# Kernel optimization log

Measured on AMD Instinct MI355X. Metric: run time of the kernel, lower is better.

The kernel has to match this reference:

```python
import jax, jax.numpy as jnp
import numpy as np

IN_DIM = 2048
H1, H2 = 128, 64
LATENT = 4
KDIM = 1024
GAMMA = 1.0
THRESHOLD = 0.0
BATCH = 65536


def setup_inputs() -> dict:
    key = jax.random.key(0)
    ks = jax.random.split(key, 12)
    s = lambda fan_in: 1.0 / np.sqrt(fan_in)
    inp = {
        "x": jax.random.normal(ks[0], (BATCH, IN_DIM), dtype=jnp.float32),
        # encoder params (stored [in, out]; math x @ W + b)
        "W1": jax.random.uniform(ks[1], (IN_DIM, H1), jnp.float32, -s(IN_DIM), s(IN_DIM)),
        "b1": jnp.zeros((H1,), jnp.float32),
        "W2": jax.random.uniform(ks[2], (H1, H2), jnp.float32, -s(H1), s(H1)),
        "b2": jnp.zeros((H2,), jnp.float32),
        "W3": jax.random.uniform(ks[3], (H2, LATENT), jnp.float32, -s(H2), s(H2)),
        "b3": jnp.zeros((LATENT,), jnp.float32),
        # 2x2 conv filter (flattened kernel) + bias
        "conv_k": jax.random.uniform(ks[4], (LATENT,), jnp.float32, -0.5, 0.5),
        "conv_b": jnp.zeros((), jnp.float32),
        # RBF basis (width LATENT+1: latent features + conv scalar)
        "basis": jax.random.normal(ks[5], (KDIM, LATENT + 1), dtype=jnp.float32),
        "head_w": jax.random.uniform(ks[6], (KDIM,), jnp.float32, -s(KDIM), s(KDIM)),
        "head_b": jnp.zeros((), jnp.float32),
    }
    return inp


def reference(x, W1, b1, W2, b2, W3, b3, conv_k, conv_b, basis, head_w, head_b):
    # encoder (dropout is eval-mode identity)
    h = jax.nn.relu(x @ W1 + b1)
    h = jax.nn.relu(h @ W2 + b2)
    z = h @ W3 + b3                                  # [B, 4]
    # ConvFilter.run on the 2x2 reshape of z: a 2x2 conv over a 2x2 input is a
    # single dot product; mean over the 1x1 output is identity.
    conv_vec = jax.nn.sigmoid(z @ conv_k + conv_b - THRESHOLD)  # [B]
    z = jnp.concatenate([z, conv_vec[:, None]], axis=-1)        # [B, 5]
    # batched RBF kernel to all basis vectors: exp(-gamma * ||z_i - b_j||^2)
    sq = (jnp.sum(z * z, axis=-1, keepdims=True)
          + jnp.sum(basis * basis, axis=-1)[None, :]
          - 2.0 * (z @ basis.T))                     # [B, KDIM]
    k_mat = jnp.exp(-GAMMA * sq)
    out = k_mat @ head_w + head_b                    # [B]
    return out
```

## Files before the change

kernel.cpp:

```cpp
#include <hip/hip_runtime.h>
#include <hip/hip_bf16.h>
#include <math.h>

typedef __attribute__((ext_vector_type(8))) __bf16 bf16x8;
typedef __attribute__((ext_vector_type(4))) float f32x4;

#define IN_DIM 2048
#define NH1 128
#define NH2 64
#define KDIM 1024

__device__ inline f32x4 mfma16(bf16x8 a, bf16x8 b, f32x4 c) {
    return __builtin_amdgcn_mfma_f32_16x16x32_bf16(a, b, c, 0, 0, 0);
}

__global__ void prep_kernel(const float* __restrict__ W1,
                            const float* __restrict__ W2,
                            const float* __restrict__ basis,
                            const float* __restrict__ head_w,
                            __bf16* __restrict__ w1f,
                            __bf16* __restrict__ w2f,
                            float* __restrict__ bp) {
    int idx = blockIdx.x * 256 + threadIdx.x;
    if (idx < IN_DIM * NH1) {
        int ks = idx >> 12;
        int rem = idx & 4095;
        int c = rem >> 9;
        int q = rem & 511;
        int l = q >> 3, e = q & 7;
        int k = ks * 32 + ((l >> 4) << 3) + e;
        int col = (c << 4) + (l & 15);
        w1f[idx] = (__bf16)W1[k * NH1 + col];
    }
    if (idx < NH1 * NH2) {
        int cb = idx >> 9;
        int c2 = cb >> 2, kb = cb & 3;
        int q = idx & 511;
        int l = q >> 3, e = q & 7;
        int k = kb * 32 + ((l >> 4) << 3) + e;
        int col = (c2 << 4) + (l & 15);
        w2f[idx] = (__bf16)W2[k * NH2 + col];
    }
    if (idx < KDIM) {
        const float* b = basis + idx * 5;
        float n2 = b[0]*b[0] + b[1]*b[1] + b[2]*b[2] + b[3]*b[3] + b[4]*b[4];
        float* o = bp + idx * 8;
        o[0] = b[0]; o[1] = b[1]; o[2] = b[2]; o[3] = b[3]; o[4] = b[4];
        o[5] = 1.0f;
        o[6] = head_w[idx] * expf(-n2);
        o[7] = 0.0f;
    }
}

__launch_bounds__(256)
__global__ void fused_main(const float* __restrict__ x,
                           const __bf16* __restrict__ w1f,
                           const float* __restrict__ b1,
                           const __bf16* __restrict__ w2f,
                           const float* __restrict__ b2,
                           const float* __restrict__ W3,
                           const float* __restrict__ b3,
                           const float* __restrict__ conv_k,
                           const float* __restrict__ conv_b,
                           const float* __restrict__ bp,
                           const float* __restrict__ head_b,
                           float* __restrict__ out) {
    __shared__ __bf16 h1s[4][32 * NH1];
    __shared__ float z5s[128][8];
    __shared__ float psum[128];

    const int tid = threadIdx.x;
    const int w = __builtin_amdgcn_readfirstlane(tid >> 6);
    const int l = tid & 63;
    const int row0 = blockIdx.x * 128 + w * 32;

    f32x4 acc[2][8];
#pragma unroll
    for (int g = 0; g < 2; ++g)
#pragma unroll
        for (int c = 0; c < 8; ++c) acc[g][c] = (f32x4){0.f, 0.f, 0.f, 0.f};

    const float* xw0 = x + (size_t)(row0 + (l & 15)) * IN_DIM + ((l >> 4) << 3);
    const float* xw1 = xw0 + (size_t)16 * IN_DIM;
    const __bf16* wbase = w1f + l * 8;

    for (int ks = 0; ks < 64; ++ks) {
        const float* p0 = xw0 + ks * 32;
        const float* p1 = xw1 + ks * 32;
        f32x4 a00 = *(const f32x4*)p0;
        f32x4 a01 = *(const f32x4*)(p0 + 4);
        f32x4 a10 = *(const f32x4*)p1;
        f32x4 a11 = *(const f32x4*)(p1 + 4);
        bf16x8 A0, A1;
        A0[0] = (__bf16)a00.x; A0[1] = (__bf16)a00.y; A0[2] = (__bf16)a00.z; A0[3] = (__bf16)a00.w;
        A0[4] = (__bf16)a01.x; A0[5] = (__bf16)a01.y; A0[6] = (__bf16)a01.z; A0[7] = (__bf16)a01.w;
        A1[0] = (__bf16)a10.x; A1[1] = (__bf16)a10.y; A1[2] = (__bf16)a10.z; A1[3] = (__bf16)a10.w;
        A1[4] = (__bf16)a11.x; A1[5] = (__bf16)a11.y; A1[6] = (__bf16)a11.z; A1[7] = (__bf16)a11.w;
        const __bf16* wp = wbase + ((size_t)ks << 12);
#pragma unroll
        for (int c = 0; c < 8; ++c) {
            bf16x8 B = *(const bf16x8*)(wp + (c << 9));
            acc[0][c] = mfma16(A0, B, acc[0][c]);
            acc[1][c] = mfma16(A1, B, acc[1][c]);
        }
    }

    float b1v[8];
#pragma unroll
    for (int c = 0; c < 8; ++c) b1v[c] = b1[c * 16 + (l & 15)];
    __bf16* hw1 = &h1s[w][0];
#pragma unroll
    for (int g = 0; g < 2; ++g)
#pragma unroll
        for (int c = 0; c < 8; ++c)
#pragma unroll
            for (int r = 0; r < 4; ++r) {
                int rr = g * 16 + ((l >> 4) << 2) + r;
                int cc = c * 16 + (l & 15);
                hw1[rr * NH1 + cc] = (__bf16)fmaxf(acc[g][c][r] + b1v[c], 0.f);
            }

    __syncthreads();

    f32x4 acc2[2][4];
#pragma unroll
    for (int g = 0; g < 2; ++g)
#pragma unroll
        for (int c = 0; c < 4; ++c) acc2[g][c] = (f32x4){0.f, 0.f, 0.f, 0.f};

#pragma unroll
    for (int kb = 0; kb < 4; ++kb) {
        bf16x8 A0 = *(const bf16x8*)&hw1[(l & 15) * NH1 + kb * 32 + ((l >> 4) << 3)];
        bf16x8 A1 = *(const bf16x8*)&hw1[(16 + (l & 15)) * NH1 + kb * 32 + ((l >> 4) << 3)];
#pragma unroll
        for (int c2 = 0; c2 < 4; ++c2) {
            bf16x8 B = *(const bf16x8*)(w2f + (((c2 << 2) + kb) << 9) + l * 8);
            acc2[0][c2] = mfma16(A0, B, acc2[0][c2]);
            acc2[1][c2] = mfma16(A1, B, acc2[1][c2]);
        }
    }

    float b2v[4];
#pragma unroll
    for (int c2 = 0; c2 < 4; ++c2) b2v[c2] = b2[c2 * 16 + (l & 15)];
    float w3l[4][4];
#pragma unroll
    for (int c2 = 0; c2 < 4; ++c2) {
        f32x4 t = *(const f32x4*)&W3[(c2 * 16 + (l & 15)) * 4];
        w3l[c2][0] = t.x; w3l[c2][1] = t.y; w3l[c2][2] = t.z; w3l[c2][3] = t.w;
    }
    float h2v[2][4][4];
#pragma unroll
    for (int g = 0; g < 2; ++g)
#pragma unroll
        for (int c2 = 0; c2 < 4; ++c2)
#pragma unroll
            for (int r = 0; r < 4; ++r)
                h2v[g][c2][r] = fmaxf(acc2[g][c2][r] + b2v[c2], 0.f);

    float pz[2][4][4];
#pragma unroll
    for (int g = 0; g < 2; ++g)
#pragma unroll
        for (int r = 0; r < 4; ++r)
#pragma unroll
            for (int j = 0; j < 4; ++j) {
                float s = 0.f;
#pragma unroll
                for (int c2 = 0; c2 < 4; ++c2) s = fmaf(h2v[g][c2][r], w3l[c2][j], s);
                pz[g][r][j] = s;
            }
#pragma unroll
    for (int off = 1; off < 16; off <<= 1)
#pragma unroll
        for (int g = 0; g < 2; ++g)
#pragma unroll
            for (int r = 0; r < 4; ++r)
#pragma unroll
                for (int j = 0; j < 4; ++j)
                    pz[g][r][j] += __shfl_xor(pz[g][r][j], off, 64);

    const float ck0 = conv_k[0], ck1 = conv_k[1], ck2 = conv_k[2], ck3 = conv_k[3];
    const float cbv = conv_b[0];
    const float b30 = b3[0], b31 = b3[1], b32 = b3[2], b33 = b3[3];
    const float L2E = 1.44269504088896340736f;

    if ((l & 15) == 0) {
#pragma unroll
        for (int g = 0; g < 2; ++g)
#pragma unroll
            for (int r = 0; r < 4; ++r) {
                int rl = w * 32 + g * 16 + ((l >> 4) << 2) + r;
                float z0 = pz[g][r][0] + b30;
                float z1 = pz[g][r][1] + b31;
                float z2 = pz[g][r][2] + b32;
                float z3 = pz[g][r][3] + b33;
                float s = fmaf(z0, ck0, fmaf(z1, ck1, fmaf(z2, ck2, fmaf(z3, ck3, cbv))));
                float sg = 1.f / (1.f + expf(-s));
                float n2 = z0*z0 + z1*z1 + z2*z2 + z3*z3 + sg*sg;
                z5s[rl][0] = 2.f * L2E * z0;
                z5s[rl][1] = 2.f * L2E * z1;
                z5s[rl][2] = 2.f * L2E * z2;
                z5s[rl][3] = 2.f * L2E * z3;
                z5s[rl][4] = 2.f * L2E * sg;
                z5s[rl][5] = -L2E * n2;
            }
    }
    __syncthreads();

    const int row = tid & 127;
    const int half = __builtin_amdgcn_readfirstlane(tid >> 7);
    f32x4 za = *(const f32x4*)&z5s[row][0];
    float z4s = z5s[row][4];
    float z5c = z5s[row][5];
    const float* bpp = bp + (size_t)half * 512 * 8;
    float accum = 0.f;
#pragma unroll 4
    for (int j = 0; j < 512; ++j) {
        f32x4 q0 = *(const f32x4*)&bpp[j * 8];
        f32x4 q1 = *(const f32x4*)&bpp[j * 8 + 4];
        float arg = fmaf(za.x, q0.x,
                    fmaf(za.y, q0.y,
                    fmaf(za.z, q0.z,
                    fmaf(za.w, q0.w,
                    fmaf(z4s, q1.x, z5c)))));
        accum = fmaf(q1.z, exp2f(arg), accum);
    }
    if (half) psum[row] = accum;
    __syncthreads();
    if (!half) out[blockIdx.x * 128 + row] = accum + psum[row] + head_b[0];
}

extern "C" void kernel_launch(void* const* d_in, const int* in_sizes, int n_in,
                              void* d_out, int out_size, void* d_ws, size_t ws_size,
                              hipStream_t stream) {
    const float* x     = (const float*)d_in[0];
    const float* W1    = (const float*)d_in[1];
    const float* b1    = (const float*)d_in[2];
    const float* W2    = (const float*)d_in[3];
    const float* b2    = (const float*)d_in[4];
    const float* W3    = (const float*)d_in[5];
    const float* b3    = (const float*)d_in[6];
    const float* ck    = (const float*)d_in[7];
    const float* cb    = (const float*)d_in[8];
    const float* basis = (const float*)d_in[9];
    const float* hwv   = (const float*)d_in[10];
    const float* hb    = (const float*)d_in[11];

    __bf16* w1f = (__bf16*)d_ws;
    __bf16* w2f = (__bf16*)((char*)d_ws + 524288);
    float*  bpp = (float*)((char*)d_ws + 524288 + 16384);

    prep_kernel<<<1024, 256, 0, stream>>>(W1, W2, basis, hwv, w1f, w2f, bpp);
    fused_main<<<512, 256, 0, stream>>>(x, w1f, b1, w2f, b2, W3, b3, ck, cb,
                                        bpp, hb, (float*)d_out);
}
```

Before: 194.6 us.

## Halve rows per wave, double grid, and software-prefetch x tiles in layer 1

Each wave now handles 16 rows instead of 32, so the grid grows from 512 to 1024 blocks of 64 rows. This cuts accumulator registers, and launch bounds request 4 blocks per CU for higher occupancy. The first GEMM loop is unrolled by two, with the x loads for step ks+2 issued ahead to hide global latency. The RBF stage splits the basis across all four waves with a four-way partial-sum reduction. The trade-off is that each W1 fragment loaded is now reused for half as many rows, so W1 read traffic per output doubles.

```diff
diff --git a/kernel.cpp b/kernel.cpp
--- a/kernel.cpp
+++ b/kernel.cpp
@@ -52,7 +52,27 @@
     }
 }
 
-__launch_bounds__(256)
+
+#define S1_STEP(A0, A1, KS, PF_EN, PA0, PA1, KPF)                             \
+    {                                                                         \
+        bf16x8 Af;                                                            \
+        Af[0] = (__bf16)A0.x; Af[1] = (__bf16)A0.y;                           \
+        Af[2] = (__bf16)A0.z; Af[3] = (__bf16)A0.w;                           \
+        Af[4] = (__bf16)A1.x; Af[5] = (__bf16)A1.y;                           \
+        Af[6] = (__bf16)A1.z; Af[7] = (__bf16)A1.w;                           \
+        if (PF_EN) {                                                          \
+            PA0 = *(const f32x4*)(xp + (KPF) * 32);                           \
+            PA1 = *(const f32x4*)(xp + (KPF) * 32 + 4);                       \
+        }                                                                     \
+        const __bf16* wp = wbase + ((size_t)(KS) << 12);                      \
+        _Pragma("unroll")                                                     \
+        for (int c = 0; c < 8; ++c) {                                         \
+            bf16x8 B = *(const bf16x8*)(wp + (c << 9));                       \
+            acc[c] = mfma16(Af, B, acc[c]);                                   \
+        }                                                                     \
+    }
+
+__launch_bounds__(256, 4)
 __global__ void fused_main(const float* __restrict__ x,
                            const __bf16* __restrict__ w1f,
                            const float* __restrict__ b1,
@@ -65,78 +85,60 @@
                            const float* __restrict__ bp,
                            const float* __restrict__ head_b,
                            float* __restrict__ out) {
-    __shared__ __bf16 h1s[4][32 * NH1];
-    __shared__ float z5s[128][8];
-    __shared__ float psum[128];
+    __shared__ __bf16 h1s[4][16 * NH1];
+    __shared__ __align__(16) float z5s[64][8];
+    __shared__ float psum[4][64];
 
     const int tid = threadIdx.x;
     const int w = __builtin_amdgcn_readfirstlane(tid >> 6);
     const int l = tid & 63;
-    const int row0 = blockIdx.x * 128 + w * 32;
-
-    f32x4 acc[2][8];
-#pragma unroll
-    for (int g = 0; g < 2; ++g)
-#pragma unroll
-        for (int c = 0; c < 8; ++c) acc[g][c] = (f32x4){0.f, 0.f, 0.f, 0.f};
-
-    const float* xw0 = x + (size_t)(row0 + (l & 15)) * IN_DIM + ((l >> 4) << 3);
-    const float* xw1 = xw0 + (size_t)16 * IN_DIM;
+    const int row0 = blockIdx.x * 64 + w * 16;
+
+    f32x4 acc[8];
+#pragma unroll
+    for (int c = 0; c < 8; ++c) acc[c] = (f32x4){0.f, 0.f, 0.f, 0.f};
+
+    const float* xp = x + (size_t)(row0 + (l & 15)) * IN_DIM + ((l >> 4) << 3);
     const __bf16* wbase = w1f + l * 8;
 
-    for (int ks = 0; ks < 64; ++ks) {
-        const float* p0 = xw0 + ks * 32;
-        const float* p1 = xw1 + ks * 32;
-        f32x4 a00 = *(const f32x4*)p0;
-        f32x4 a01 = *(const f32x4*)(p0 + 4);
-        f32x4 a10 = *(const f32x4*)p1;
-        f32x4 a11 = *(const f32x4*)(p1 + 4);
-        bf16x8 A0, A1;
-        A0[0] = (__bf16)a00.x; A0[1] = (__bf16)a00.y; A0[2] = (__bf16)a00.z; A0[3] = (__bf16)a00.w;
-        A0[4] = (__bf16)a01.x; A0[5] = (__bf16)a01.y; A0[6] = (__bf16)a01.z; A0[7] = (__bf16)a01.w;
-        A1[0] = (__bf16)a10.x; A1[1] = (__bf16)a10.y; A1[2] = (__bf16)a10.z; A1[3] = (__bf16)a10.w;
-        A1[4] = (__bf16)a11.x; A1[5] = (__bf16)a11.y; A1[6] = (__bf16)a11.z; A1[7] = (__bf16)a11.w;
-        const __bf16* wp = wbase + ((size_t)ks << 12);
-#pragma unroll
-        for (int c = 0; c < 8; ++c) {
-            bf16x8 B = *(const bf16x8*)(wp + (c << 9));
-            acc[0][c] = mfma16(A0, B, acc[0][c]);
-            acc[1][c] = mfma16(A1, B, acc[1][c]);
-        }
-    }
+    f32x4 aA0 = *(const f32x4*)(xp);
+    f32x4 aA1 = *(const f32x4*)(xp + 4);
+    f32x4 aB0 = *(const f32x4*)(xp + 32);
+    f32x4 aB1 = *(const f32x4*)(xp + 36);
+
+    for (int ks = 0; ks < 62; ks += 2) {
+        S1_STEP(aA0, aA1, ks,     1, aA0, aA1, ks + 2)
+        S1_STEP(aB0, aB1, ks + 1, 1, aB0, aB1, ks + 3)
+    }
+    S1_STEP(aA0, aA1, 62, 0, aA0, aA1, 0)
+    S1_STEP(aB0, aB1, 63, 0, aB0, aB1, 0)
 
     float b1v[8];
 #pragma unroll
     for (int c = 0; c < 8; ++c) b1v[c] = b1[c * 16 + (l & 15)];
     __bf16* hw1 = &h1s[w][0];
 #pragma unroll
-    for (int g = 0; g < 2; ++g)
-#pragma unroll
-        for (int c = 0; c < 8; ++c)
-#pragma unroll
-            for (int r = 0; r < 4; ++r) {
-                int rr = g * 16 + ((l >> 4) << 2) + r;
-                int cc = c * 16 + (l & 15);
-                hw1[rr * NH1 + cc] = (__bf16)fmaxf(acc[g][c][r] + b1v[c], 0.f);
-            }
+    for (int c = 0; c < 8; ++c)
+#pragma unroll
+        for (int r = 0; r < 4; ++r) {
+            int rr = ((l >> 4) << 2) + r;
+            int cc = c * 16 + (l & 15);
+            hw1[rr * NH1 + cc] = (__bf16)fmaxf(acc[c][r] + b1v[c], 0.f);
+        }
 
     __syncthreads();
 
-    f32x4 acc2[2][4];
-#pragma unroll
-    for (int g = 0; g < 2; ++g)
-#pragma unroll
-        for (int c = 0; c < 4; ++c) acc2[g][c] = (f32x4){0.f, 0.f, 0.f, 0.f};
+    f32x4 acc2[4];
+#pragma unroll
+    for (int c2 = 0; c2 < 4; ++c2) acc2[c2] = (f32x4){0.f, 0.f, 0.f, 0.f};
 
 #pragma unroll
     for (int kb = 0; kb < 4; ++kb) {
-        bf16x8 A0 = *(const bf16x8*)&hw1[(l & 15) * NH1 + kb * 32 + ((l >> 4) << 3)];
-        bf16x8 A1 = *(const bf16x8*)&hw1[(16 + (l & 15)) * NH1 + kb * 32 + ((l >> 4) << 3)];
+        bf16x8 A = *(const bf16x8*)&hw1[(l & 15) * NH1 + kb * 32 + ((l >> 4) << 3)];
 #pragma unroll
         for (int c2 = 0; c2 < 4; ++c2) {
             bf16x8 B = *(const bf16x8*)(w2f + (((c2 << 2) + kb) << 9) + l * 8);
-            acc2[0][c2] = mfma16(A0, B, acc2[0][c2]);
-            acc2[1][c2] = mfma16(A1, B, acc2[1][c2]);
+            acc2[c2] = mfma16(A, B, acc2[c2]);
         }
     }
 
@@ -149,36 +151,30 @@
         f32x4 t = *(const f32x4*)&W3[(c2 * 16 + (l & 15)) * 4];
         w3l[c2][0] = t.x; w3l[c2][1] = t.y; w3l[c2][2] = t.z; w3l[c2][3] = t.w;
     }
-    float h2v[2][4][4];
-#pragma unroll
-    for (int g = 0; g < 2; ++g)
-#pragma unroll
-        for (int c2 = 0; c2 < 4; ++c2)
-#pragma unroll
-            for (int r = 0; r < 4; ++r)
-                h2v[g][c2][r] = fmaxf(acc2[g][c2][r] + b2v[c2], 0.f);
-
-    float pz[2][4][4];
-#pragma unroll
-    for (int g = 0; g < 2; ++g)
+    float h2v[4][4];
+#pragma unroll
+    for (int c2 = 0; c2 < 4; ++c2)
 #pragma unroll
         for (int r = 0; r < 4; ++r)
-#pragma unroll
-            for (int j = 0; j < 4; ++j) {
-                float s = 0.f;
-#pragma unroll
-                for (int c2 = 0; c2 < 4; ++c2) s = fmaf(h2v[g][c2][r], w3l[c2][j], s);
-                pz[g][r][j] = s;
-            }
+            h2v[c2][r] = fmaxf(acc2[c2][r] + b2v[c2], 0.f);
+
+    float pz[4][4];
+#pragma unroll
+    for (int r = 0; r < 4; ++r)
+#pragma unroll
+        for (int j = 0; j < 4; ++j) {
+            float s = 0.f;
+#pragma unroll
+            for (int c2 = 0; c2 < 4; ++c2) s = fmaf(h2v[c2][r], w3l[c2][j], s);
+            pz[r][j] = s;
+        }
 #pragma unroll
     for (int off = 1; off < 16; off <<= 1)
 #pragma unroll
-        for (int g = 0; g < 2; ++g)
-#pragma unroll
-            for (int r = 0; r < 4; ++r)
-#pragma unroll
-                for (int j = 0; j < 4; ++j)
-                    pz[g][r][j] += __shfl_xor(pz[g][r][j], off, 64);
+        for (int r = 0; r < 4; ++r)
+#pragma unroll
+            for (int j = 0; j < 4; ++j)
+                pz[r][j] += __shfl_xor(pz[r][j], off, 64);
 
     const float ck0 = conv_k[0], ck1 = conv_k[1], ck2 = conv_k[2], ck3 = conv_k[3];
     const float cbv = conv_b[0];
@@ -187,36 +183,32 @@
 
     if ((l & 15) == 0) {
 #pragma unroll
-        for (int g = 0; g < 2; ++g)
-#pragma unroll
-            for (int r = 0; r < 4; ++r) {
-                int rl = w * 32 + g * 16 + ((l >> 4) << 2) + r;
-                float z0 = pz[g][r][0] + b30;
-                float z1 = pz[g][r][1] + b31;
-                float z2 = pz[g][r][2] + b32;
-                float z3 = pz[g][r][3] + b33;
-                float s = fmaf(z0, ck0, fmaf(z1, ck1, fmaf(z2, ck2, fmaf(z3, ck3, cbv))));
-                float sg = 1.f / (1.f + expf(-s));
-                float n2 = z0*z0 + z1*z1 + z2*z2 + z3*z3 + sg*sg;
-                z5s[rl][0] = 2.f * L2E * z0;
-                z5s[rl][1] = 2.f * L2E * z1;
-                z5s[rl][2] = 2.f * L2E * z2;
-                z5s[rl][3] = 2.f * L2E * z3;
-                z5s[rl][4] = 2.f * L2E * sg;
-                z5s[rl][5] = -L2E * n2;
-            }
+        for (int r = 0; r < 4; ++r) {
+            int rl = w * 16 + ((l >> 4) << 2) + r;
+            float z0 = pz[r][0] + b30;
+            float z1 = pz[r][1] + b31;
+            float z2 = pz[r][2] + b32;
+            float z3 = pz[r][3] + b33;
+            float s = fmaf(z0, ck0, fmaf(z1, ck1, fmaf(z2, ck2, fmaf(z3, ck3, cbv))));
+            float sg = 1.f / (1.f + expf(-s));
+            float n2 = z0*z0 + z1*z1 + z2*z2 + z3*z3 + sg*sg;
+            z5s[rl][0] = 2.f * L2E * z0;
+            z5s[rl][1] = 2.f * L2E * z1;
+            z5s[rl][2] = 2.f * L2E * z2;
+            z5s[rl][3] = 2.f * L2E * z3;
+            z5s[rl][4] = 2.f * L2E * sg;
+            z5s[rl][5] = -L2E * n2;
+        }
     }
     __syncthreads();
 
-    const int row = tid & 127;
-    const int half = __builtin_amdgcn_readfirstlane(tid >> 7);
-    f32x4 za = *(const f32x4*)&z5s[row][0];
-    float z4s = z5s[row][4];
-    float z5c = z5s[row][5];
-    const float* bpp = bp + (size_t)half * 512 * 8;
+    f32x4 za = *(const f32x4*)&z5s[l][0];
+    float z4s = z5s[l][4];
+    float z5c = z5s[l][5];
+    const float* bpp = bp + (size_t)w * 256 * 8;
     float accum = 0.f;
 #pragma unroll 4
-    for (int j = 0; j < 512; ++j) {
+    for (int j = 0; j < 256; ++j) {
         f32x4 q0 = *(const f32x4*)&bpp[j * 8];
         f32x4 q1 = *(const f32x4*)&bpp[j * 8 + 4];
         float arg = fmaf(za.x, q0.x,
@@ -226,9 +218,11 @@
                     fmaf(z4s, q1.x, z5c)))));
         accum = fmaf(q1.z, exp2f(arg), accum);
     }
-    if (half) psum[row] = accum;
+    psum[w][l] = accum;
     __syncthreads();
-    if (!half) out[blockIdx.x * 128 + row] = accum + psum[row] + head_b[0];
+    if (w == 0)
+        out[blockIdx.x * 64 + l] =
+            psum[0][l] + psum[1][l] + psum[2][l] + psum[3][l] + head_b[0];
 }
 
 extern "C" void kernel_launch(void* const* d_in, const int* in_sizes, int n_in,
@@ -252,6 +246,6 @@
     float*  bpp = (float*)((char*)d_ws + 524288 + 16384);
 
     prep_kernel<<<1024, 256, 0, stream>>>(W1, W2, basis, hwv, w1f, w2f, bpp);
-    fused_main<<<512, 256, 0, stream>>>(x, w1f, b1, w2f, b2, W3, b3, ck, cb,
-                                        bpp, hb, (float*)d_out);
-}
+    fused_main<<<1024, 256, 0, stream>>>(x, w1f, b1, w2f, b2, W3, b3, ck, cb,
+                                         bpp, hb, (float*)d_out);
+}
```

Result: slower. 275.0 us (+41.3%).

## Stage x and W1 tiles through LDS with a triple-buffered async load pipeline

Applied to the files above, without the earlier changes.

The first GEMM layer now loads x and W1 tiles into shared memory with global_load_lds in a three-stage ring buffer, waiting with vmcnt counts and barriers so loads for later k-steps overlap the MFMA work on the current one. x tiles use an XOR swizzle to avoid LDS bank conflicts. All shared arrays are folded into one 72KB buffer that is reused for the h1, z5 and psum scratch. The large LDS footprint reduces the number of blocks that fit on a CU, and the hand-written waitcnt/barrier schedule is fragile.

```diff
diff --git a/kernel.cpp b/kernel.cpp
--- a/kernel.cpp
+++ b/kernel.cpp
@@ -12,6 +12,12 @@
 
 __device__ inline f32x4 mfma16(bf16x8 a, bf16x8 b, f32x4 c) {
     return __builtin_amdgcn_mfma_f32_16x16x32_bf16(a, b, c, 0, 0, 0);
+}
+
+__device__ inline void gld16(const void* g, void* l) {
+    __builtin_amdgcn_global_load_lds(
+        (const __attribute__((address_space(1))) void*)g,
+        (__attribute__((address_space(3))) void*)l, 16, 0, 0);
 }
 
 __global__ void prep_kernel(const float* __restrict__ W1,
@@ -65,14 +71,39 @@
                            const float* __restrict__ bp,
                            const float* __restrict__ head_b,
                            float* __restrict__ out) {
-    __shared__ __bf16 h1s[4][32 * NH1];
-    __shared__ float z5s[128][8];
-    __shared__ float psum[128];
+    __shared__ __align__(16) char smem[73728];
 
     const int tid = threadIdx.x;
-    const int w = __builtin_amdgcn_readfirstlane(tid >> 6);
+    const int w = tid >> 6;
     const int l = tid & 63;
-    const int row0 = blockIdx.x * 128 + w * 32;
+    const int r = l & 15;
+    const int j = l >> 4;
+    const int row0 = blockIdx.x * 128;
+
+    const float* aSrc[4];
+#pragma unroll
+    for (int q = 0; q < 4; ++q)
+        aSrc[q] = x + (size_t)(row0 + w * 32 + q * 8 + (l >> 3)) * IN_DIM
+                    + (((l & 7) ^ (l >> 3)) << 2);
+    const __bf16* bSrc[2];
+#pragma unroll
+    for (int q = 0; q < 2; ++q)
+        bSrc[q] = w1f + (w * 2 + q) * 512 + l * 8;
+
+#define STAGE_ISSUE(AO, BO)                                                   \
+    {                                                                         \
+        _Pragma("unroll")                                                     \
+        for (int q = 0; q < 4; ++q)                                           \
+            gld16(aSrc[q], smem + (AO) + (w * 32 + q * 8) * 128);             \
+        _Pragma("unroll")                                                     \
+        for (int q = 0; q < 2; ++q)                                           \
+            gld16(bSrc[q], smem + (BO) + (w * 2 + q) * 1024);                 \
+    }
+#define ADVANCE()                                                             \
+    {                                                                         \
+        _Pragma("unroll") for (int q = 0; q < 4; ++q) aSrc[q] += 32;          \
+        _Pragma("unroll") for (int q = 0; q < 2; ++q) bSrc[q] += 4096;        \
+    }
 
     f32x4 acc[2][8];
 #pragma unroll
@@ -80,58 +111,86 @@
 #pragma unroll
         for (int c = 0; c < 8; ++c) acc[g][c] = (f32x4){0.f, 0.f, 0.f, 0.f};
 
-    const float* xw0 = x + (size_t)(row0 + (l & 15)) * IN_DIM + ((l >> 4) << 3);
-    const float* xw1 = xw0 + (size_t)16 * IN_DIM;
-    const __bf16* wbase = w1f + l * 8;
-
-    for (int ks = 0; ks < 64; ++ks) {
-        const float* p0 = xw0 + ks * 32;
-        const float* p1 = xw1 + ks * 32;
-        f32x4 a00 = *(const f32x4*)p0;
-        f32x4 a01 = *(const f32x4*)(p0 + 4);
-        f32x4 a10 = *(const f32x4*)p1;
-        f32x4 a11 = *(const f32x4*)(p1 + 4);
-        bf16x8 A0, A1;
-        A0[0] = (__bf16)a00.x; A0[1] = (__bf16)a00.y; A0[2] = (__bf16)a00.z; A0[3] = (__bf16)a00.w;
-        A0[4] = (__bf16)a01.x; A0[5] = (__bf16)a01.y; A0[6] = (__bf16)a01.z; A0[7] = (__bf16)a01.w;
-        A1[0] = (__bf16)a10.x; A1[1] = (__bf16)a10.y; A1[2] = (__bf16)a10.z; A1[3] = (__bf16)a10.w;
-        A1[4] = (__bf16)a11.x; A1[5] = (__bf16)a11.y; A1[6] = (__bf16)a11.z; A1[7] = (__bf16)a11.w;
-        const __bf16* wp = wbase + ((size_t)ks << 12);
-#pragma unroll
-        for (int c = 0; c < 8; ++c) {
-            bf16x8 B = *(const bf16x8*)(wp + (c << 9));
-            acc[0][c] = mfma16(A0, B, acc[0][c]);
-            acc[1][c] = mfma16(A1, B, acc[1][c]);
-        }
-    }
+#define KSTEP(AO, BO)                                                         \
+    {                                                                         \
+        bf16x8 Bv[8];                                                         \
+        _Pragma("unroll")                                                     \
+        for (int c = 0; c < 8; ++c)                                           \
+            Bv[c] = *(const bf16x8*)(smem + (BO) + (c << 10) + l * 16);       \
+        _Pragma("unroll")                                                     \
+        for (int g = 0; g < 2; ++g) {                                         \
+            const char* ab = smem + (AO) + (w * 32 + g * 16 + r) * 128;       \
+            f32x4 f0 = *(const f32x4*)(ab + (((2 * j)     ^ (r & 7)) << 4));  \
+            f32x4 f1 = *(const f32x4*)(ab + (((2 * j + 1) ^ (r & 7)) << 4));  \
+            bf16x8 Af;                                                        \
+            Af[0] = (__bf16)f0.x; Af[1] = (__bf16)f0.y;                       \
+            Af[2] = (__bf16)f0.z; Af[3] = (__bf16)f0.w;                       \
+            Af[4] = (__bf16)f1.x; Af[5] = (__bf16)f1.y;                       \
+            Af[6] = (__bf16)f1.z; Af[7] = (__bf16)f1.w;                       \
+            _Pragma("unroll")                                                 \
+            for (int c = 0; c < 8; ++c)                                       \
+                acc[g][c] = mfma16(Af, Bv[c], acc[g][c]);                     \
+        }                                                                     \
+    }
+
+    STAGE_ISSUE(0, 49152)      ADVANCE()
+    STAGE_ISSUE(16384, 57344)  ADVANCE()
+    STAGE_ISSUE(32768, 65536)  ADVANCE()
+    asm volatile("s_waitcnt vmcnt(12)" ::: "memory");
+    __builtin_amdgcn_s_barrier();
+    __builtin_amdgcn_sched_barrier(0);
+
+    unsigned aoff = 0, boff = 49152;
+#pragma unroll 1
+    for (int t = 0; t < 61; ++t) {
+        KSTEP(aoff, boff)
+        STAGE_ISSUE(aoff, boff)
+        ADVANCE()
+        asm volatile("s_waitcnt vmcnt(12)" ::: "memory");
+        __builtin_amdgcn_s_barrier();
+        __builtin_amdgcn_sched_barrier(0);
+        aoff = (aoff == 32768u) ? 0u : aoff + 16384u;
+        boff = (boff == 65536u) ? 49152u : boff + 8192u;
+    }
+    KSTEP(aoff, boff)
+    asm volatile("s_waitcnt vmcnt(6)" ::: "memory");
+    __builtin_amdgcn_s_barrier();
+    __builtin_amdgcn_sched_barrier(0);
+    aoff = (aoff == 32768u) ? 0u : aoff + 16384u;
+    boff = (boff == 65536u) ? 49152u : boff + 8192u;
+    KSTEP(aoff, boff)
+    asm volatile("s_waitcnt vmcnt(0)" ::: "memory");
+    __builtin_amdgcn_s_barrier();
+    __builtin_amdgcn_sched_barrier(0);
+    aoff = (aoff == 32768u) ? 0u : aoff + 16384u;
+    boff = (boff == 65536u) ? 49152u : boff + 8192u;
+    KSTEP(aoff, boff)
+
+    __syncthreads();
 
     float b1v[8];
 #pragma unroll
-    for (int c = 0; c < 8; ++c) b1v[c] = b1[c * 16 + (l & 15)];
-    __bf16* hw1 = &h1s[w][0];
+    for (int c = 0; c < 8; ++c) b1v[c] = b1[c * 16 + r];
+    __bf16* hw1 = (__bf16*)(smem + w * 8192);
+#pragma unroll
+    for (int c = 0; c < 8; ++c)
+#pragma unroll
+        for (int g = 0; g < 2; ++g)
+#pragma unroll
+            for (int rr = 0; rr < 4; ++rr)
+                hw1[(g * 16 + j * 4 + rr) * NH1 + c * 16 + r] =
+                    (__bf16)fmaxf(acc[g][c][rr] + b1v[c], 0.f);
+
+    f32x4 acc2[2][4];
 #pragma unroll
     for (int g = 0; g < 2; ++g)
 #pragma unroll
-        for (int c = 0; c < 8; ++c)
-#pragma unroll
-            for (int r = 0; r < 4; ++r) {
-                int rr = g * 16 + ((l >> 4) << 2) + r;
-                int cc = c * 16 + (l & 15);
-                hw1[rr * NH1 + cc] = (__bf16)fmaxf(acc[g][c][r] + b1v[c], 0.f);
-            }
-
-    __syncthreads();
-
-    f32x4 acc2[2][4];
-#pragma unroll
-    for (int g = 0; g < 2; ++g)
-#pragma unroll
-        for (int c = 0; c < 4; ++c) acc2[g][c] = (f32x4){0.f, 0.f, 0.f, 0.f};
+        for (int c2 = 0; c2 < 4; ++c2) acc2[g][c2] = (f32x4){0.f, 0.f, 0.f, 0.f};
 
 #pragma unroll
     for (int kb = 0; kb < 4; ++kb) {
-        bf16x8 A0 = *(const bf16x8*)&hw1[(l & 15) * NH1 + kb * 32 + ((l >> 4) << 3)];
-        bf16x8 A1 = *(const bf16x8*)&hw1[(16 + (l & 15)) * NH1 + kb * 32 + ((l >> 4) << 3)];
+        bf16x8 A0 = *(const bf16x8*)&hw1[r * NH1 + kb * 32 + j * 8];
+        bf16x8 A1 = *(const bf16x8*)&hw1[(16 + r) * NH1 + kb * 32 + j * 8];
 #pragma unroll
         for (int c2 = 0; c2 < 4; ++c2) {
             bf16x8 B = *(const bf16x8*)(w2f + (((c2 << 2) + kb) << 9) + l * 8);
@@ -142,11 +201,11 @@
 
     float b2v[4];
 #pragma unroll
-    for (int c2 = 0; c2 < 4; ++c2) b2v[c2] = b2[c2 * 16 + (l & 15)];
+    for (int c2 = 0; c2 < 4; ++c2) b2v[c2] = b2[c2 * 16 + r];
     float w3l[4][4];
 #pragma unroll
     for (int c2 = 0; c2 < 4; ++c2) {
-        f32x4 t = *(const f32x4*)&W3[(c2 * 16 + (l & 15)) * 4];
+        f32x4 t = *(const f32x4*)&W3[(c2 * 16 + r) * 4];
         w3l[c2][0] = t.x; w3l[c2][1] = t.y; w3l[c2][2] = t.z; w3l[c2][3] = t.w;
     }
     float h2v[2][4][4];
@@ -155,46 +214,50 @@
 #pragma unroll
         for (int c2 = 0; c2 < 4; ++c2)
 #pragma unroll
-            for (int r = 0; r < 4; ++r)
-                h2v[g][c2][r] = fmaxf(acc2[g][c2][r] + b2v[c2], 0.f);
+            for (int rr = 0; rr < 4; ++rr)
+                h2v[g][c2][rr] = fmaxf(acc2[g][c2][rr] + b2v[c2], 0.f);
 
     float pz[2][4][4];
 #pragma unroll
     for (int g = 0; g < 2; ++g)
 #pragma unroll
-        for (int r = 0; r < 4; ++r)
-#pragma unroll
-            for (int j = 0; j < 4; ++j) {
+        for (int rr = 0; rr < 4; ++rr)
+#pragma unroll
+            for (int jj = 0; jj < 4; ++jj) {
                 float s = 0.f;
 #pragma unroll
-                for (int c2 = 0; c2 < 4; ++c2) s = fmaf(h2v[g][c2][r], w3l[c2][j], s);
-                pz[g][r][j] = s;
+                for (int c2 = 0; c2 < 4; ++c2)
+                    s = fmaf(h2v[g][c2][rr], w3l[c2][jj], s);
+                pz[g][rr][jj] = s;
             }
 #pragma unroll
     for (int off = 1; off < 16; off <<= 1)
 #pragma unroll
         for (int g = 0; g < 2; ++g)
 #pragma unroll
-            for (int r = 0; r < 4; ++r)
-#pragma unroll
-                for (int j = 0; j < 4; ++j)
-                    pz[g][r][j] += __shfl_xor(pz[g][r][j], off, 64);
+            for (int rr = 0; rr < 4; ++rr)
+#pragma unroll
+                for (int jj = 0; jj < 4; ++jj)
+                    pz[g][rr][jj] += __shfl_xor(pz[g][rr][jj], off, 64);
 
     const float ck0 = conv_k[0], ck1 = conv_k[1], ck2 = conv_k[2], ck3 = conv_k[3];
     const float cbv = conv_b[0];
     const float b30 = b3[0], b31 = b3[1], b32 = b3[2], b33 = b3[3];
     const float L2E = 1.44269504088896340736f;
 
-    if ((l & 15) == 0) {
+    float (*z5s)[8] = (float(*)[8])(smem + 49152);
+    float* psum = (float*)(smem + 53248);
+
+    if (r == 0) {
 #pragma unroll
         for (int g = 0; g < 2; ++g)
 #pragma unroll
-            for (int r = 0; r < 4; ++r) {
-                int rl = w * 32 + g * 16 + ((l >> 4) << 2) + r;
-                float z0 = pz[g][r][0] + b30;
-                float z1 = pz[g][r][1] + b31;
-                float z2 = pz[g][r][2] + b32;
-                float z3 = pz[g][r][3] + b33;
+            for (int rr = 0; rr < 4; ++rr) {
+                int rl = w * 32 + g * 16 + (j << 2) + rr;
+                float z0 = pz[g][rr][0] + b30;
+                float z1 = pz[g][rr][1] + b31;
+                float z2 = pz[g][rr][2] + b32;
+                float z3 = pz[g][rr][3] + b33;
                 float s = fmaf(z0, ck0, fmaf(z1, ck1, fmaf(z2, ck2, fmaf(z3, ck3, cbv))));
                 float sg = 1.f / (1.f + expf(-s));
                 float n2 = z0*z0 + z1*z1 + z2*z2 + z3*z3 + sg*sg;
@@ -209,16 +272,16 @@
     __syncthreads();
 
     const int row = tid & 127;
-    const int half = __builtin_amdgcn_readfirstlane(tid >> 7);
+    const int half = tid >> 7;
     f32x4 za = *(const f32x4*)&z5s[row][0];
     float z4s = z5s[row][4];
     float z5c = z5s[row][5];
     const float* bpp = bp + (size_t)half * 512 * 8;
     float accum = 0.f;
 #pragma unroll 4
-    for (int j = 0; j < 512; ++j) {
-        f32x4 q0 = *(const f32x4*)&bpp[j * 8];
-        f32x4 q1 = *(const f32x4*)&bpp[j * 8 + 4];
+    for (int jb = 0; jb < 512; ++jb) {
+        f32x4 q0 = *(const f32x4*)&bpp[jb * 8];
+        f32x4 q1 = *(const f32x4*)&bpp[jb * 8 + 4];
         float arg = fmaf(za.x, q0.x,
                     fmaf(za.y, q0.y,
                     fmaf(za.z, q0.z,
```

New measurement: 172.3 us. -11.5%, faster.
